# Optimization experiments

Measured on AMD Instinct MI355X. Metric: run time of the kernel, lower is better.

Reference implementation:

```python
import jax, jax.numpy as jnp
import numpy as np

N_NODES = 100_000
N_EDGES = 1_000_000
H = 128
NUM_STATES = 4
UPPER_T, LOWER_T, NUM_ITERS, TEMP_EVAL = 1.0, 0.1, 10000, 0.1


def temp_by_step(step, upper, lower, num_iters, temp_eval):
    # Python-level schedule: eval temp at step == -1, else linear anneal.
    if step == -1:
        return temp_eval
    frac = min(step / num_iters, 1.0)
    return upper + (lower - upper) * frac


def from_binary_states(states):
    # [*, k] bits -> integer id in [0, 2**k)
    weights = 2 ** jnp.arange(states.shape[-1])
    return (states * weights).sum(-1)


def setup_inputs() -> dict:
    key = jax.random.key(0)
    ks = jax.random.split(key, 20)
    N, E, h = N_NODES, N_EDGES, H
    node_states = jax.random.randint(ks[0], (N, NUM_STATES), 0, 2)
    edge_states = jax.random.randint(ks[1], (E, NUM_STATES), 0, 2)
    scalars = jax.random.normal(ks[2], (E, 1), jnp.float32)
    # first N edges are self-loops ordered by node id (required by the module's
    # node_scalars = scalars[src == dst] indexing convention)
    loops = jnp.arange(N)
    src = jax.random.randint(ks[3], (E - N,), 0, N)
    dst = jax.random.randint(ks[4], (E - N,), 0, N)
    dst = jnp.where(dst == src, (dst + 1) % N, dst)  # no accidental self-loops
    edge_index = jnp.stack([jnp.concatenate([loops, src]),
                            jnp.concatenate([loops, dst])])
    batched_reverse_idx = jax.random.randint(ks[5], (E,), 0, E)
    batch_scalars = jax.random.normal(ks[6], (E, 1, 1), jnp.float32)
    s = 0.02
    params = dict(
        node_emb=s * jax.random.normal(ks[7], (2 ** NUM_STATES, h), jnp.float32),
        edge_emb=s * jax.random.normal(ks[8], (2 ** NUM_STATES, h), jnp.float32),
        combine_W=s * jax.random.normal(ks[9], (2 * h, h), jnp.float32),
        combine_b=jnp.zeros((h,), jnp.float32),
        keep_W=s * jax.random.normal(ks[10], (h, 2), jnp.float32),
        keep_b=jnp.zeros((2,), jnp.float32),
        push_W=s * jax.random.normal(ks[11], (h, 2), jnp.float32),
        push_b=jnp.zeros((2,), jnp.float32),
        push_node_W=s * jax.random.normal(ks[12], (h, 2), jnp.float32),
        push_node_b=jnp.zeros((2,), jnp.float32),
        increment_W=s * jax.random.normal(ks[13], (h, 2), jnp.float32),
        increment_b=jnp.zeros((2,), jnp.float32),
    )
    return dict(node_states=node_states, edge_states=edge_states, scalars=scalars,
                edge_index=edge_index, batched_reverse_idx=batched_reverse_idx,
                batch_scalars=batch_scalars, processor_step=0, training_step=0,
                **params)


def reference(node_states, edge_states, scalars, edge_index, batched_reverse_idx,
              batch_scalars, processor_step, training_step,
              node_emb, edge_emb, combine_W, combine_b, keep_W, keep_b,
              push_W, push_b, push_node_W, push_node_b,
              increment_W, increment_b):
    N = node_states.shape[0]
    tau = temp_by_step(int(training_step), UPPER_T, LOWER_T, NUM_ITERS, TEMP_EVAL)
    # use_noise = config.use_noise (False) and training_step != -1 -> False

    node_fts = node_emb[from_binary_states(node_states)]   # [N, h]
    edge_fts = edge_emb[from_binary_states(edge_states)]   # [E, h]
    src, dst = edge_index[0], edge_index[1]
    fts = jnp.concatenate([edge_fts[batched_reverse_idx], node_fts[src]], axis=1)
    fts = fts @ combine_W + combine_b                       # [E, h]

    s = scalars.reshape(-1)                                 # [E]

    def pair_gumbel_first(W, b):
        # grouped (per-edge pair) softmax; take first component (== [::2])
        logits = (fts @ W + b) / tau                        # [E, 2]
        return jax.nn.softmax(logits, axis=-1)[:, 0]

    increment = 1.0 * pair_gumbel_first(increment_W, increment_b)
    keep = s * pair_gumbel_first(keep_W, keep_b)

    # push: first N edges are self-loops, self-loop of node i is edge i
    push_wo = pair_gumbel_first(push_W, push_b)
    push_w = pair_gumbel_first(push_node_W, push_node_b)
    node_scalars = s[:N]                                    # scalars at self-loops
    s_wo = s - node_scalars[dst]
    s_w = s_wo + node_scalars[src]
    acc = (jax.ops.segment_sum(push_wo * s_wo, dst, num_segments=N)
           + jax.ops.segment_sum(push_w * s_w, dst, num_segments=N))  # [N]
    edge_push = jnp.zeros_like(s).at[:N].set(acc)           # nonzero only on self-loops

    new_scalars = (increment + keep + edge_push)[:, None]   # [E, 1]
    target = batch_scalars[:, processor_step]               # [E, 1]
    loss = jnp.mean((target - new_scalars) ** 2)
    return new_scalars, loss
```

## Files before the change

### kernel.cpp

```cpp
#include <hip/hip_runtime.h>
#include <math.h>

#define N_NODES 100000
#define N_EDGES 1000000
#define HDIM 128
#define N_NONLOOP (N_EDGES - N_NODES)

typedef float  vfloat2 __attribute__((ext_vector_type(2)));
typedef float  vfloat4 __attribute__((ext_vector_type(4)));

__device__ __forceinline__ float get_invtau(const int* __restrict__ training_step) {
    int step = training_step[0];
    float tau;
    if (step == -1) {
        tau = 0.1f;
    } else {
        float frac = fminf((float)step / 10000.0f, 1.0f);
        tau = 1.0f + (0.1f - 1.0f) * frac;
    }
    return 1.0f / tau;
}

__device__ __forceinline__ float wave_reduce(float v) {
    #pragma unroll
    for (int off = 32; off > 0; off >>= 1) v += __shfl_down(v, off, 64);
    return v;
}

__global__ void tab_stage1(const float* __restrict__ cW,
                           const float* __restrict__ kW, const float* __restrict__ pW,
                           const float* __restrict__ pnW, const float* __restrict__ iW,
                           const int* __restrict__ tstep,
                           float* __restrict__ uv)
{
    __shared__ float wd[512];
    const float invtau = get_invtau(tstep);
    for (int i = threadIdx.x; i < 512; i += 256) {
        const int h = i >> 7, d = i & 127;
        const float* W = (h == 0) ? kW : (h == 1) ? pW : (h == 2) ? pnW : iW;
        wd[i] = W[2 * d] - W[2 * d + 1];
    }
    __syncthreads();

    const int row  = blockIdx.x * 4 + (threadIdx.x >> 6);
    const int lane = threadIdx.x & 63;
    const int half = row >> 9;
    const int r    = row & 511;
    const int h    = r >> 7, d = r & 127;
    const int cwrow = half * 128 + d;

    float p = cW[cwrow * 128 + lane]      * wd[h * 128 + lane]
            + cW[cwrow * 128 + 64 + lane] * wd[h * 128 + 64 + lane];
    p = wave_reduce(p);
    if (lane == 0) uv[row] = p * invtau;
}

__global__ void tab_stage2(const float* __restrict__ node_emb,
                           const float* __restrict__ edge_emb,
                           const float* __restrict__ cb,
                           const float* __restrict__ kW, const float* __restrict__ kb,
                           const float* __restrict__ pW, const float* __restrict__ pb,
                           const float* __restrict__ pnW, const float* __restrict__ pnb,
                           const float* __restrict__ iW, const float* __restrict__ ib,
                           const int* __restrict__ tstep,
                           const float* __restrict__ uv,
                           float* __restrict__ tabs)
{
    const int w = blockIdx.x * 4 + (threadIdx.x >> 6);
    if (w >= 132) return;
    const int lane = threadIdx.x & 63;
    const float invtau = get_invtau(tstep);

    float p;
    if (w < 128) {
        const int isB = w >> 6, h = (w >> 4) & 3, i = w & 15;
        const float* emb = isB ? node_emb : edge_emb;
        const float* uvp = uv + isB * 512 + h * 128;
        p = emb[i * 128 + lane] * uvp[lane] + emb[i * 128 + 64 + lane] * uvp[64 + lane];
    } else {
        const int h = w - 128;
        const float* W = (h == 0) ? kW : (h == 1) ? pW : (h == 2) ? pnW : iW;
        p = cb[lane]      * (W[2 * lane] - W[2 * lane + 1])
          + cb[64 + lane] * (W[2 * (64 + lane)] - W[2 * (64 + lane) + 1]);
    }
    p = wave_reduce(p);
    if (lane == 0) {
        if (w < 64) {
            const int h = (w >> 4) & 3, i = w & 15;
            tabs[i * 4 + h] = p;
        } else if (w < 128) {
            const int h = (w >> 4) & 3, i = w & 15;
            tabs[64 + i * 4 + h] = p;
        } else {
            const int h = w - 128;
            const float* b = (h == 0) ? kb : (h == 1) ? pb : (h == 2) ? pnb : ib;
            tabs[128 + h] = (p + b[0] - b[1]) * invtau;
        }
    }
}

__global__ void precompute(const int* __restrict__ node_states,
                           const int* __restrict__ edge_states,
                           const float* __restrict__ s,
                           unsigned char* __restrict__ es_idx,
                           float2* __restrict__ node_pack,
                           float* __restrict__ acc,
                           float* __restrict__ loss_out)
{
    const int e = blockIdx.x * blockDim.x + threadIdx.x;
    if (e < N_EDGES) {
        int4 st = ((const int4*)edge_states)[e];
        es_idx[e] = (unsigned char)(st.x + 2 * st.y + 4 * st.z + 8 * st.w);
    }
    if (e < N_NODES) {
        int4 st = ((const int4*)node_states)[e];
        const int idx = st.x + 2 * st.y + 4 * st.z + 8 * st.w;
        float2 np;
        np.x = s[e];
        np.y = __int_as_float(idx);
        node_pack[e] = np;
        acc[e] = 0.f;
    }
    if (e == 0) *loss_out = 0.f;
}

__global__ __launch_bounds__(256) void edge_kernel(
    const float* __restrict__ s,
    const int* __restrict__ src,
    const int* __restrict__ dst,
    const int* __restrict__ brev,
    const unsigned char* __restrict__ es_idx,
    const float2* __restrict__ node_pack,
    const float* __restrict__ tabs,
    const float* __restrict__ target,
    float* __restrict__ acc,
    float* __restrict__ out,
    float* __restrict__ loss_out)
{
    __shared__ float4 sf[33];
    if (threadIdx.x < 33) sf[threadIdx.x] = ((const float4*)tabs)[threadIdx.x];
    __syncthreads();

    const int t = blockIdx.x * blockDim.x + threadIdx.x;
    float lsum = 0.f;

    if (t < N_NONLOOP / 4) {
        const int g = (N_NODES / 4) + t;
        const int4   rv = ((const int4*)brev)[g];
        const int4   sr = ((const int4*)src)[g];
        const int4   ds = ((const int4*)dst)[g];
        const float4 sv = ((const float4*)s)[g];
        const vfloat4 tg = __builtin_nontemporal_load(&((const vfloat4*)target)[g]);

        const int rvv[4] = {rv.x, rv.y, rv.z, rv.w};
        const int srv[4] = {sr.x, sr.y, sr.z, sr.w};
        const int dsv[4] = {ds.x, ds.y, ds.z, ds.w};
        const float svv[4] = {sv.x, sv.y, sv.z, sv.w};
        const float tgv[4] = {tg.x, tg.y, tg.z, tg.w};

        int ei[4];
        float2 np[4];
        float sd[4];
        #pragma unroll
        for (int j = 0; j < 4; ++j) {
            ei[j] = es_idx[rvv[j]];
            np[j] = node_pack[srv[j]];
            sd[j] = node_pack[dsv[j]].x;
        }

        const float4 c4 = sf[32];
        float ov[4];
        #pragma unroll
        for (int j = 0; j < 4; ++j) {
            const int   ni = __float_as_int(np[j].y);
            const float ss = np[j].x;
            const float4 a = sf[ei[j]];
            const float4 b = sf[16 + ni];
            const float lk  = a.x + b.x + c4.x;
            const float lp  = a.y + b.y + c4.y;
            const float lpn = a.z + b.z + c4.z;
            const float li  = a.w + b.w + c4.w;
            const float pk  = 1.f / (1.f + __expf(-lk));
            const float pp  = 1.f / (1.f + __expf(-lp));
            const float ppn = 1.f / (1.f + __expf(-lpn));
            const float pi  = 1.f / (1.f + __expf(-li));

            const float s_wo = svv[j] - sd[j];
            const float s_w  = s_wo + ss;
            unsafeAtomicAdd(&acc[dsv[j]], pp * s_wo + ppn * s_w);

            ov[j] = pi + svv[j] * pk;
            const float d = tgv[j] - ov[j];
            lsum += d * d;
        }
        vfloat4 o4 = {ov[0], ov[1], ov[2], ov[3]};
        __builtin_nontemporal_store(o4, &((vfloat4*)out)[g]);
    }

    lsum = wave_reduce(lsum);
    __shared__ float wsum[4];
    const int lane = threadIdx.x & 63, wid = threadIdx.x >> 6;
    if (lane == 0) wsum[wid] = lsum;
    __syncthreads();
    if (threadIdx.x == 0) {
        const float tot = wsum[0] + wsum[1] + wsum[2] + wsum[3];
        atomicAdd(loss_out, tot * (1.0f / (float)N_EDGES));
    }
}

__global__ __launch_bounds__(256) void finalize_nodes(
    const int* __restrict__ brev,
    const unsigned char* __restrict__ es_idx,
    const float2* __restrict__ node_pack,
    const float* __restrict__ tabs,
    const float* __restrict__ target,
    const float* __restrict__ acc,
    float* __restrict__ out,
    float* __restrict__ loss_out)
{
    __shared__ float4 sf[33];
    if (threadIdx.x < 33) sf[threadIdx.x] = ((const float4*)tabs)[threadIdx.x];
    __syncthreads();

    const int n = blockIdx.x * blockDim.x + threadIdx.x;
    float sq = 0.f;
    if (n < N_NODES) {
        const int    rev = brev[n];
        const int    ei  = es_idx[rev];
        const float2 np  = node_pack[n];
        const int    ni  = __float_as_int(np.y);
        const float  sv  = np.x;

        const float4 a = sf[ei];
        const float4 b = sf[16 + ni];
        const float4 c4 = sf[32];
        const float lk  = a.x + b.x + c4.x;
        const float lpn = a.z + b.z + c4.z;
        const float li  = a.w + b.w + c4.w;
        const float pk  = 1.f / (1.f + __expf(-lk));
        const float ppn = 1.f / (1.f + __expf(-lpn));
        const float pi  = 1.f / (1.f + __expf(-li));

        const float v = pi + sv * (pk + ppn) + acc[n];
        out[n] = v;
        const float d = target[n] - v;
        sq = d * d;
    }
    sq = wave_reduce(sq);
    __shared__ float wsum[4];
    const int lane = threadIdx.x & 63, wid = threadIdx.x >> 6;
    if (lane == 0) wsum[wid] = sq;
    __syncthreads();
    if (threadIdx.x == 0) {
        const float tot = wsum[0] + wsum[1] + wsum[2] + wsum[3];
        atomicAdd(loss_out, tot * (1.0f / (float)N_EDGES));
    }
}

extern "C" void kernel_launch(void* const* d_in, const int* in_sizes, int n_in,
                              void* d_out, int out_size, void* d_ws, size_t ws_size,
                              hipStream_t stream) {
    const int*   node_states   = (const int*)d_in[0];
    const int*   edge_states   = (const int*)d_in[1];
    const float* scalars       = (const float*)d_in[2];
    const int*   edge_index    = (const int*)d_in[3];
    const int*   brev          = (const int*)d_in[4];
    const float* batch_scalars = (const float*)d_in[5];
    const int*   training_step = (const int*)d_in[7];
    const float* node_emb  = (const float*)d_in[8];
    const float* edge_emb  = (const float*)d_in[9];
    const float* combine_W = (const float*)d_in[10];
    const float* combine_b = (const float*)d_in[11];
    const float* keep_W  = (const float*)d_in[12];
    const float* keep_b  = (const float*)d_in[13];
    const float* push_W  = (const float*)d_in[14];
    const float* push_b  = (const float*)d_in[15];
    const float* pushn_W = (const float*)d_in[16];
    const float* pushn_b = (const float*)d_in[17];
    const float* inc_W   = (const float*)d_in[18];
    const float* inc_b   = (const float*)d_in[19];

    float* out = (float*)d_out;

    char* ws = (char*)d_ws;
    float*  tabs = (float*)ws;
    float*  uv   = (float*)(ws + 1024);
    float*  acc  = (float*)(ws + 1024 + 4096);
    float2* node_pack = (float2*)(ws + 1024 + 4096 + (size_t)N_NODES * 4);
    unsigned char* es_idx = (unsigned char*)(ws + 1024 + 4096 + (size_t)N_NODES * 12);

    const int* srcp = edge_index;
    const int* dstp = edge_index + N_EDGES;

    tab_stage1<<<256, 256, 0, stream>>>(combine_W, keep_W, push_W, pushn_W, inc_W,
                                        training_step, uv);
    tab_stage2<<<33, 256, 0, stream>>>(node_emb, edge_emb, combine_b,
                                       keep_W, keep_b, push_W, push_b,
                                       pushn_W, pushn_b, inc_W, inc_b,
                                       training_step, uv, tabs);

    precompute<<<(N_EDGES + 255) / 256, 256, 0, stream>>>(node_states, edge_states,
                                                          scalars, es_idx, node_pack,
                                                          acc, out + N_EDGES);

    const int ethreads = N_NONLOOP / 4;
    edge_kernel<<<(ethreads + 255) / 256, 256, 0, stream>>>(
        scalars, srcp, dstp, brev, es_idx, node_pack, tabs, batch_scalars,
        acc, out, out + N_EDGES);

    finalize_nodes<<<(N_NODES + 255) / 256, 256, 0, stream>>>(
        brev, es_idx, node_pack, tabs, batch_scalars, acc, out, out + N_EDGES);
}
```

Before: 179.3 us.

## Fuse precompute with first table stage and use one edge per thread

Merges the precompute kernel and the first table-building stage into one launch, with the first 256 blocks doing the weight-projection work, which removes one kernel launch. The edge kernel goes from four edges per thread with vector loads to one edge per thread with scalar loads and a scalar nontemporal store. This gives more threads and more memory parallelism for the random gathers and atomics, but drops the 128-bit coalesced loads and stores and quadruples the per-block loss reductions and atomics. The __syncthreads inside the blockIdx-guarded branch is uniform per block, so it is safe.

```diff
diff --git a/kernel.cpp b/kernel.cpp
--- a/kernel.cpp
+++ b/kernel.cpp
@@ -6,7 +6,6 @@
 #define HDIM 128
 #define N_NONLOOP (N_EDGES - N_NODES)
 
-typedef float  vfloat2 __attribute__((ext_vector_type(2)));
 typedef float  vfloat4 __attribute__((ext_vector_type(4)));
 
 __device__ __forceinline__ float get_invtau(const int* __restrict__ training_step) {
@@ -27,32 +26,58 @@
     return v;
 }
 
-__global__ void tab_stage1(const float* __restrict__ cW,
-                           const float* __restrict__ kW, const float* __restrict__ pW,
-                           const float* __restrict__ pnW, const float* __restrict__ iW,
-                           const int* __restrict__ tstep,
-                           float* __restrict__ uv)
-{
-    __shared__ float wd[512];
-    const float invtau = get_invtau(tstep);
-    for (int i = threadIdx.x; i < 512; i += 256) {
-        const int h = i >> 7, d = i & 127;
-        const float* W = (h == 0) ? kW : (h == 1) ? pW : (h == 2) ? pnW : iW;
-        wd[i] = W[2 * d] - W[2 * d + 1];
-    }
-    __syncthreads();
-
-    const int row  = blockIdx.x * 4 + (threadIdx.x >> 6);
-    const int lane = threadIdx.x & 63;
-    const int half = row >> 9;
-    const int r    = row & 511;
-    const int h    = r >> 7, d = r & 127;
-    const int cwrow = half * 128 + d;
-
-    float p = cW[cwrow * 128 + lane]      * wd[h * 128 + lane]
-            + cW[cwrow * 128 + 64 + lane] * wd[h * 128 + 64 + lane];
-    p = wave_reduce(p);
-    if (lane == 0) uv[row] = p * invtau;
+__global__ __launch_bounds__(256) void precompute_tab1(
+    const int* __restrict__ node_states,
+    const int* __restrict__ edge_states,
+    const float* __restrict__ s,
+    const float* __restrict__ cW,
+    const float* __restrict__ kW, const float* __restrict__ pW,
+    const float* __restrict__ pnW, const float* __restrict__ iW,
+    const int* __restrict__ tstep,
+    unsigned char* __restrict__ es_idx,
+    float2* __restrict__ node_pack,
+    float* __restrict__ acc,
+    float* __restrict__ loss_out,
+    float* __restrict__ uv)
+{
+    const int e = blockIdx.x * blockDim.x + threadIdx.x;
+    if (e < N_EDGES) {
+        int4 st = ((const int4*)edge_states)[e];
+        es_idx[e] = (unsigned char)(st.x + 2 * st.y + 4 * st.z + 8 * st.w);
+    }
+    if (e < N_NODES) {
+        int4 st = ((const int4*)node_states)[e];
+        const int idx = st.x + 2 * st.y + 4 * st.z + 8 * st.w;
+        float2 np;
+        np.x = s[e];
+        np.y = __int_as_float(idx);
+        node_pack[e] = np;
+        acc[e] = 0.f;
+    }
+    if (e == 0) *loss_out = 0.f;
+
+    if (blockIdx.x < 256) {
+        __shared__ float wd[512];
+        const float invtau = get_invtau(tstep);
+        for (int i = threadIdx.x; i < 512; i += 256) {
+            const int h = i >> 7, d = i & 127;
+            const float* W = (h == 0) ? kW : (h == 1) ? pW : (h == 2) ? pnW : iW;
+            wd[i] = W[2 * d] - W[2 * d + 1];
+        }
+        __syncthreads();
+
+        const int row  = blockIdx.x * 4 + (threadIdx.x >> 6);
+        const int lane = threadIdx.x & 63;
+        const int half = row >> 9;
+        const int r    = row & 511;
+        const int h    = r >> 7, d = r & 127;
+        const int cwrow = half * 128 + d;
+
+        float p = cW[cwrow * 128 + lane]      * wd[h * 128 + lane]
+                + cW[cwrow * 128 + 64 + lane] * wd[h * 128 + 64 + lane];
+        p = wave_reduce(p);
+        if (lane == 0) uv[row] = p * invtau;
+    }
 }
 
 __global__ void tab_stage2(const float* __restrict__ node_emb,
@@ -99,31 +124,6 @@
     }
 }
 
-__global__ void precompute(const int* __restrict__ node_states,
-                           const int* __restrict__ edge_states,
-                           const float* __restrict__ s,
-                           unsigned char* __restrict__ es_idx,
-                           float2* __restrict__ node_pack,
-                           float* __restrict__ acc,
-                           float* __restrict__ loss_out)
-{
-    const int e = blockIdx.x * blockDim.x + threadIdx.x;
-    if (e < N_EDGES) {
-        int4 st = ((const int4*)edge_states)[e];
-        es_idx[e] = (unsigned char)(st.x + 2 * st.y + 4 * st.z + 8 * st.w);
-    }
-    if (e < N_NODES) {
-        int4 st = ((const int4*)node_states)[e];
-        const int idx = st.x + 2 * st.y + 4 * st.z + 8 * st.w;
-        float2 np;
-        np.x = s[e];
-        np.y = __int_as_float(idx);
-        node_pack[e] = np;
-        acc[e] = 0.f;
-    }
-    if (e == 0) *loss_out = 0.f;
-}
-
 __global__ __launch_bounds__(256) void edge_kernel(
     const float* __restrict__ s,
     const int* __restrict__ src,
@@ -144,57 +144,41 @@
     const int t = blockIdx.x * blockDim.x + threadIdx.x;
     float lsum = 0.f;
 
-    if (t < N_NONLOOP / 4) {
-        const int g = (N_NODES / 4) + t;
-        const int4   rv = ((const int4*)brev)[g];
-        const int4   sr = ((const int4*)src)[g];
-        const int4   ds = ((const int4*)dst)[g];
-        const float4 sv = ((const float4*)s)[g];
-        const vfloat4 tg = __builtin_nontemporal_load(&((const vfloat4*)target)[g]);
-
-        const int rvv[4] = {rv.x, rv.y, rv.z, rv.w};
-        const int srv[4] = {sr.x, sr.y, sr.z, sr.w};
-        const int dsv[4] = {ds.x, ds.y, ds.z, ds.w};
-        const float svv[4] = {sv.x, sv.y, sv.z, sv.w};
-        const float tgv[4] = {tg.x, tg.y, tg.z, tg.w};
-
-        int ei[4];
-        float2 np[4];
-        float sd[4];
-        #pragma unroll
-        for (int j = 0; j < 4; ++j) {
-            ei[j] = es_idx[rvv[j]];
-            np[j] = node_pack[srv[j]];
-            sd[j] = node_pack[dsv[j]].x;
-        }
-
+    if (t < N_NONLOOP) {
+        const int e = N_NODES + t;
+        const int rev = brev[e];
+        const int si  = src[e];
+        const int di  = dst[e];
+        const float sv = s[e];
+        const float tg = target[e];
+
+        const int    ei = es_idx[rev];
+        const float2 np = node_pack[si];
+        const float  sd = node_pack[di].x;
+
+        const int   ni = __float_as_int(np.y);
+        const float ss = np.x;
+
+        const float4 a  = sf[ei];
+        const float4 b  = sf[16 + ni];
         const float4 c4 = sf[32];
-        float ov[4];
-        #pragma unroll
-        for (int j = 0; j < 4; ++j) {
-            const int   ni = __float_as_int(np[j].y);
-            const float ss = np[j].x;
-            const float4 a = sf[ei[j]];
-            const float4 b = sf[16 + ni];
-            const float lk  = a.x + b.x + c4.x;
-            const float lp  = a.y + b.y + c4.y;
-            const float lpn = a.z + b.z + c4.z;
-            const float li  = a.w + b.w + c4.w;
-            const float pk  = 1.f / (1.f + __expf(-lk));
-            const float pp  = 1.f / (1.f + __expf(-lp));
-            const float ppn = 1.f / (1.f + __expf(-lpn));
-            const float pi  = 1.f / (1.f + __expf(-li));
-
-            const float s_wo = svv[j] - sd[j];
-            const float s_w  = s_wo + ss;
-            unsafeAtomicAdd(&acc[dsv[j]], pp * s_wo + ppn * s_w);
-
-            ov[j] = pi + svv[j] * pk;
-            const float d = tgv[j] - ov[j];
-            lsum += d * d;
-        }
-        vfloat4 o4 = {ov[0], ov[1], ov[2], ov[3]};
-        __builtin_nontemporal_store(o4, &((vfloat4*)out)[g]);
+        const float lk  = a.x + b.x + c4.x;
+        const float lp  = a.y + b.y + c4.y;
+        const float lpn = a.z + b.z + c4.z;
+        const float li  = a.w + b.w + c4.w;
+        const float pk  = 1.f / (1.f + __expf(-lk));
+        const float pp  = 1.f / (1.f + __expf(-lp));
+        const float ppn = 1.f / (1.f + __expf(-lpn));
+        const float pi  = 1.f / (1.f + __expf(-li));
+
+        const float s_wo = sv - sd;
+        const float s_w  = s_wo + ss;
+        unsafeAtomicAdd(&acc[di], pp * s_wo + ppn * s_w);
+
+        const float ov = pi + sv * pk;
+        __builtin_nontemporal_store(ov, &out[e]);
+        const float d = tg - ov;
+        lsum += d * d;
     }
 
     lsum = wave_reduce(lsum);
@@ -292,19 +276,17 @@
     const int* srcp = edge_index;
     const int* dstp = edge_index + N_EDGES;
 
-    tab_stage1<<<256, 256, 0, stream>>>(combine_W, keep_W, push_W, pushn_W, inc_W,
-                                        training_step, uv);
+    precompute_tab1<<<(N_EDGES + 255) / 256, 256, 0, stream>>>(
+        node_states, edge_states, scalars,
+        combine_W, keep_W, push_W, pushn_W, inc_W, training_step,
+        es_idx, node_pack, acc, out + N_EDGES, uv);
+
     tab_stage2<<<33, 256, 0, stream>>>(node_emb, edge_emb, combine_b,
                                        keep_W, keep_b, push_W, push_b,
                                        pushn_W, pushn_b, inc_W, inc_b,
                                        training_step, uv, tabs);
 
-    precompute<<<(N_EDGES + 255) / 256, 256, 0, stream>>>(node_states, edge_states,
-                                                          scalars, es_idx, node_pack,
-                                                          acc, out + N_EDGES);
-
-    const int ethreads = N_NONLOOP / 4;
-    edge_kernel<<<(ethreads + 255) / 256, 256, 0, stream>>>(
+    edge_kernel<<<(N_NONLOOP + 255) / 256, 256, 0, stream>>>(
         scalars, srcp, dstp, brev, es_idx, node_pack, tabs, batch_scalars,
         acc, out, out + N_EDGES);
 
```

After: 193.2 us. 7.8% more time.

## Drop edge-state index precompute; gather int4 edge states directly in edge kernels

Applied to the files above, without the earlier changes.

Removes the separate per-edge pass that packed edge_states into a byte index and instead gathers the int4 edge-state row at the reversed index inside the edge and node kernels. The node-side precompute is merged into the first table-stage kernel, cutting one launch. This avoids a full 16 MB streaming read plus a 1 MB write, but turns a 1-byte random gather into a 16-byte random gather per edge, which raises scattered memory traffic.

```diff
diff --git a/kernel.cpp b/kernel.cpp
--- a/kernel.cpp
+++ b/kernel.cpp
@@ -6,7 +6,6 @@
 #define HDIM 128
 #define N_NONLOOP (N_EDGES - N_NODES)
 
-typedef float  vfloat2 __attribute__((ext_vector_type(2)));
 typedef float  vfloat4 __attribute__((ext_vector_type(4)));
 
 __device__ __forceinline__ float get_invtau(const int* __restrict__ training_step) {
@@ -27,32 +26,52 @@
     return v;
 }
 
-__global__ void tab_stage1(const float* __restrict__ cW,
-                           const float* __restrict__ kW, const float* __restrict__ pW,
-                           const float* __restrict__ pnW, const float* __restrict__ iW,
-                           const int* __restrict__ tstep,
-                           float* __restrict__ uv)
+__global__ __launch_bounds__(256) void precompute_tab1(
+    const int* __restrict__ node_states,
+    const float* __restrict__ s,
+    const float* __restrict__ cW,
+    const float* __restrict__ kW, const float* __restrict__ pW,
+    const float* __restrict__ pnW, const float* __restrict__ iW,
+    const int* __restrict__ tstep,
+    float2* __restrict__ node_pack,
+    float* __restrict__ acc,
+    float* __restrict__ loss_out,
+    float* __restrict__ uv)
 {
-    __shared__ float wd[512];
-    const float invtau = get_invtau(tstep);
-    for (int i = threadIdx.x; i < 512; i += 256) {
-        const int h = i >> 7, d = i & 127;
-        const float* W = (h == 0) ? kW : (h == 1) ? pW : (h == 2) ? pnW : iW;
-        wd[i] = W[2 * d] - W[2 * d + 1];
-    }
-    __syncthreads();
-
-    const int row  = blockIdx.x * 4 + (threadIdx.x >> 6);
-    const int lane = threadIdx.x & 63;
-    const int half = row >> 9;
-    const int r    = row & 511;
-    const int h    = r >> 7, d = r & 127;
-    const int cwrow = half * 128 + d;
-
-    float p = cW[cwrow * 128 + lane]      * wd[h * 128 + lane]
-            + cW[cwrow * 128 + 64 + lane] * wd[h * 128 + 64 + lane];
-    p = wave_reduce(p);
-    if (lane == 0) uv[row] = p * invtau;
+    const int n = blockIdx.x * blockDim.x + threadIdx.x;
+    if (n < N_NODES) {
+        int4 st = ((const int4*)node_states)[n];
+        const int idx = st.x + 2 * st.y + 4 * st.z + 8 * st.w;
+        float2 np;
+        np.x = s[n];
+        np.y = __int_as_float(idx);
+        node_pack[n] = np;
+        acc[n] = 0.f;
+    }
+    if (n == 0) *loss_out = 0.f;
+
+    if (blockIdx.x < 256) {
+        __shared__ float wd[512];
+        const float invtau = get_invtau(tstep);
+        for (int i = threadIdx.x; i < 512; i += 256) {
+            const int h = i >> 7, d = i & 127;
+            const float* W = (h == 0) ? kW : (h == 1) ? pW : (h == 2) ? pnW : iW;
+            wd[i] = W[2 * d] - W[2 * d + 1];
+        }
+        __syncthreads();
+
+        const int row  = blockIdx.x * 4 + (threadIdx.x >> 6);
+        const int lane = threadIdx.x & 63;
+        const int half = row >> 9;
+        const int r    = row & 511;
+        const int h    = r >> 7, d = r & 127;
+        const int cwrow = half * 128 + d;
+
+        float p = cW[cwrow * 128 + lane]      * wd[h * 128 + lane]
+                + cW[cwrow * 128 + 64 + lane] * wd[h * 128 + 64 + lane];
+        p = wave_reduce(p);
+        if (lane == 0) uv[row] = p * invtau;
+    }
 }
 
 __global__ void tab_stage2(const float* __restrict__ node_emb,
@@ -99,37 +118,12 @@
     }
 }
 
-__global__ void precompute(const int* __restrict__ node_states,
-                           const int* __restrict__ edge_states,
-                           const float* __restrict__ s,
-                           unsigned char* __restrict__ es_idx,
-                           float2* __restrict__ node_pack,
-                           float* __restrict__ acc,
-                           float* __restrict__ loss_out)
-{
-    const int e = blockIdx.x * blockDim.x + threadIdx.x;
-    if (e < N_EDGES) {
-        int4 st = ((const int4*)edge_states)[e];
-        es_idx[e] = (unsigned char)(st.x + 2 * st.y + 4 * st.z + 8 * st.w);
-    }
-    if (e < N_NODES) {
-        int4 st = ((const int4*)node_states)[e];
-        const int idx = st.x + 2 * st.y + 4 * st.z + 8 * st.w;
-        float2 np;
-        np.x = s[e];
-        np.y = __int_as_float(idx);
-        node_pack[e] = np;
-        acc[e] = 0.f;
-    }
-    if (e == 0) *loss_out = 0.f;
-}
-
 __global__ __launch_bounds__(256) void edge_kernel(
     const float* __restrict__ s,
     const int* __restrict__ src,
     const int* __restrict__ dst,
     const int* __restrict__ brev,
-    const unsigned char* __restrict__ es_idx,
+    const int* __restrict__ edge_states,
     const float2* __restrict__ node_pack,
     const float* __restrict__ tabs,
     const float* __restrict__ target,
@@ -158,12 +152,12 @@
         const float svv[4] = {sv.x, sv.y, sv.z, sv.w};
         const float tgv[4] = {tg.x, tg.y, tg.z, tg.w};
 
-        int ei[4];
+        int4  es[4];
         float2 np[4];
         float sd[4];
         #pragma unroll
         for (int j = 0; j < 4; ++j) {
-            ei[j] = es_idx[rvv[j]];
+            es[j] = ((const int4*)edge_states)[rvv[j]];
             np[j] = node_pack[srv[j]];
             sd[j] = node_pack[dsv[j]].x;
         }
@@ -172,9 +166,10 @@
         float ov[4];
         #pragma unroll
         for (int j = 0; j < 4; ++j) {
+            const int ei = es[j].x + 2 * es[j].y + 4 * es[j].z + 8 * es[j].w;
             const int   ni = __float_as_int(np[j].y);
             const float ss = np[j].x;
-            const float4 a = sf[ei[j]];
+            const float4 a = sf[ei];
             const float4 b = sf[16 + ni];
             const float lk  = a.x + b.x + c4.x;
             const float lp  = a.y + b.y + c4.y;
@@ -210,7 +205,7 @@
 
 __global__ __launch_bounds__(256) void finalize_nodes(
     const int* __restrict__ brev,
-    const unsigned char* __restrict__ es_idx,
+    const int* __restrict__ edge_states,
     const float2* __restrict__ node_pack,
     const float* __restrict__ tabs,
     const float* __restrict__ target,
@@ -226,7 +221,8 @@
     float sq = 0.f;
     if (n < N_NODES) {
         const int    rev = brev[n];
-        const int    ei  = es_idx[rev];
+        const int4   est = ((const int4*)edge_states)[rev];
+        const int    ei  = est.x + 2 * est.y + 4 * est.z + 8 * est.w;
         const float2 np  = node_pack[n];
         const int    ni  = __float_as_int(np.y);
         const float  sv  = np.x;
@@ -287,27 +283,25 @@
     float*  uv   = (float*)(ws + 1024);
     float*  acc  = (float*)(ws + 1024 + 4096);
     float2* node_pack = (float2*)(ws + 1024 + 4096 + (size_t)N_NODES * 4);
-    unsigned char* es_idx = (unsigned char*)(ws + 1024 + 4096 + (size_t)N_NODES * 12);
 
     const int* srcp = edge_index;
     const int* dstp = edge_index + N_EDGES;
 
-    tab_stage1<<<256, 256, 0, stream>>>(combine_W, keep_W, push_W, pushn_W, inc_W,
-                                        training_step, uv);
+    precompute_tab1<<<(N_NODES + 255) / 256, 256, 0, stream>>>(
+        node_states, scalars,
+        combine_W, keep_W, push_W, pushn_W, inc_W, training_step,
+        node_pack, acc, out + N_EDGES, uv);
+
     tab_stage2<<<33, 256, 0, stream>>>(node_emb, edge_emb, combine_b,
                                        keep_W, keep_b, push_W, push_b,
                                        pushn_W, pushn_b, inc_W, inc_b,
                                        training_step, uv, tabs);
 
-    precompute<<<(N_EDGES + 255) / 256, 256, 0, stream>>>(node_states, edge_states,
-                                                          scalars, es_idx, node_pack,
-                                                          acc, out + N_EDGES);
-
     const int ethreads = N_NONLOOP / 4;
     edge_kernel<<<(ethreads + 255) / 256, 256, 0, stream>>>(
-        scalars, srcp, dstp, brev, es_idx, node_pack, tabs, batch_scalars,
+        scalars, srcp, dstp, brev, edge_states, node_pack, tabs, batch_scalars,
         acc, out, out + N_EDGES);
 
     finalize_nodes<<<(N_NODES + 255) / 256, 256, 0, stream>>>(
-        brev, es_idx, node_pack, tabs, batch_scalars, acc, out, out + N_EDGES);
-}
+        brev, edge_states, node_pack, tabs, batch_scalars, acc, out, out + N_EDGES);
+}
```

Result: no change. 177.5 us (-1.0%).
